# Kernel optimization log

Hardware: AMD Instinct MI355X
Metric: run time of the kernel (lower is better)

## Reference

```python
import jax, jax.numpy as jnp
import numpy as np
import math

B = 2048
NOSC = 64            # oscillators per modality
M = 3                # modalities (audio, text, vision) in sorted order
BDIM = 256           # binding_dim
DT = 0.01
NSTEPS = 10
DIMS = [512, 768, 1024]  # audio, text, vision
TWO_PI = 2.0 * math.pi


def setup_inputs() -> dict:
    key = jax.random.key(0)
    ks = iter(jax.random.split(key, 40))
    d = {}
    names = ['a', 't', 'v']
    for name, dim, x_key in zip(names, DIMS, ['x_audio', 'x_text', 'x_vision']):
        d[x_key] = jax.random.normal(next(ks), (B, dim), dtype=jnp.float32)
        s = 1.0 / math.sqrt(dim)
        d[f'Wf_{name}'] = jax.random.uniform(next(ks), (BDIM, dim), jnp.float32, -s, s)
        d[f'bf_{name}'] = jax.random.uniform(next(ks), (BDIM,), jnp.float32, -s, s)
        d[f'Wp_{name}'] = jax.random.uniform(next(ks), (NOSC, dim), jnp.float32, -s, s)
        d[f'bp_{name}'] = jax.random.uniform(next(ks), (NOSC,), jnp.float32, -s, s)
    # omegas: randn*0.1 + 1.0 + i*0.5 for i-th sorted modality
    for i, name in enumerate(names):
        d[f'omega_{name}'] = jax.random.normal(next(ks), (NOSC,), jnp.float32) * 0.1 + 1.0 + i * 0.5
    N = M * NOSC
    d['inter_coupling'] = jax.random.normal(next(ks), (N, N), jnp.float32) * 0.1
    s = 1.0 / math.sqrt(BDIM * M)
    d['W_fusion'] = jax.random.uniform(next(ks), (BDIM, BDIM * M), jnp.float32, -s, s)
    d['b_fusion'] = jax.random.uniform(next(ks), (BDIM,), jnp.float32, -s, s)
    return d


def reference(x_audio, x_text, x_vision,
              Wf_a, bf_a, Wp_a, bp_a,
              Wf_t, bf_t, Wp_t, bp_t,
              Wf_v, bf_v, Wp_v, bp_v,
              omega_a, omega_t, omega_v,
              inter_coupling, W_fusion, b_fusion):
    def enc(x, Wf, bf, Wp, bp):
        encoded = x @ Wf.T + bf                       # (B, BDIM)
        phases = (x @ Wp.T + bp) % TWO_PI             # (B, NOSC)
        return encoded, phases

    e_a, p_a = enc(x_audio, Wf_a, bf_a, Wp_a, bp_a)
    e_t, p_t = enc(x_text, Wf_t, bf_t, Wp_t, bp_t)
    e_v, p_v = enc(x_vision, Wf_v, bf_v, Wp_v, bp_v)

    phases = jnp.concatenate([p_a, p_t, p_v], axis=-1)        # (B, N)
    omega = jnp.concatenate([omega_a, omega_t, omega_v])      # (N,)
    K = (inter_coupling + inter_coupling.T) * 0.5             # (N, N)
    N = phases.shape[-1]

    def step(ph, _):
        diff = ph[:, :, None] - ph[:, None, :]                # (B, N, N)
        forces = jnp.einsum('ij,bij->bi', K, jnp.sin(diff)) / N
        ph = (ph + DT * (omega[None, :] + forces)) % TWO_PI
        return ph, None

    phases, _ = jax.lax.scan(step, phases, None, length=NSTEPS)

    pm = [phases[:, i * NOSC:(i + 1) * NOSC] for i in range(M)]  # per-modality

    # PLV between banks a,b: |mean_{i,j} exp(i(a_i - b_j))| = R_a * R_b where
    # R = |mean_k exp(i phi_k)| (resultant length), computed with real math.
    R = jnp.stack([jnp.sqrt(jnp.mean(jnp.cos(p), -1) ** 2 +
                            jnp.mean(jnp.sin(p), -1) ** 2) for p in pm])  # (M, B)
    bm = jnp.mean(R[:, None, :] * R[None, :, :], axis=-1)      # (M, M)
    binding_matrix = jnp.where(jnp.eye(M, dtype=bool), 1.0, bm)

    fused_parts = []
    for e, p in zip([e_a, e_t, e_v], pm):
        phase_mod = jnp.mean(jnp.cos(p), axis=-1, keepdims=True)  # (B, 1)
        fused_parts.append(e * (0.5 + 0.5 * phase_mod))
    fused = jnp.concatenate(fused_parts, axis=-1)              # (B, M*BDIM)
    bound = fused @ W_fusion.T + b_fusion                      # (B, BDIM)

    triu = jnp.triu(jnp.ones((M, M), dtype=bool), k=1)
    total = jnp.sum(jnp.where(triu, binding_matrix, 0.0)) / triu.sum()
    total_binding = jnp.full((bound.shape[0],), total)

    return bound, binding_matrix, phases, total_binding
```

## Files before the change

kernel.cpp:

```cpp
#include <hip/hip_runtime.h>
#include <math.h>

typedef short bf16x8 __attribute__((ext_vector_type(8)));
typedef short bf16x4 __attribute__((ext_vector_type(4)));
typedef float f32x4  __attribute__((ext_vector_type(4)));

#define INV_2PI  0.15915494309189535f
#define TWO_PI_F 6.283185307179586f
#define FSCALE   8.2893199e-06f

static __device__ inline short f2bf(float f) {
    union { float f; unsigned u; } v; v.f = f;
    unsigned r = (v.u + 0x7FFFu + ((v.u >> 16) & 1u)) >> 16;
    return (short)r;
}
static __device__ inline float bf2f(short h) {
    union { unsigned u; float f; } v; v.u = ((unsigned)(unsigned short)h) << 16;
    return v.f;
}

__global__ __launch_bounds__(256) void front_kernel(
    const float* __restrict__ xa, const float* __restrict__ xt, const float* __restrict__ xv,
    const float* __restrict__ Wpa, const float* __restrict__ Wpt, const float* __restrict__ Wpv,
    const float* __restrict__ Wfa, const float* __restrict__ Wft, const float* __restrict__ Wfv,
    const float* __restrict__ Wfu,
    const float* __restrict__ IC,
    const float* __restrict__ oa, const float* __restrict__ ot, const float* __restrict__ ov,
    const float* __restrict__ bpa, const float* __restrict__ bpt, const float* __restrict__ bpv,
    float* __restrict__ partial, short* __restrict__ XB, short* __restrict__ WB,
    short* __restrict__ Kp,
    float* __restrict__ om_eff, float* __restrict__ bp_all, float* __restrict__ bacc)
{
    __shared__ alignas(16) char smem[13056];
    int b = blockIdx.x;
    int t = threadIdx.x;

    if (b < 288) {
        float (*As)[136] = (float (*)[136])smem;
        float (*Bs)[68]  = (float (*)[68])(smem + 8704);
        int slot = b % 18, rb = b / 18;
        int z = slot < 4 ? 0 : (slot < 10 ? 1 : 2);
        int chunk = slot - (z == 0 ? 0 : (z == 1 ? 4 : 10));
        const float* A = z == 0 ? xa : (z == 1 ? xt : xv);
        const float* W = z == 0 ? Wpa : (z == 1 ? Wpt : Wpv);
        int K = z == 0 ? 512 : (z == 1 ? 768 : 1024);
        int kb = chunk * 128;
        int m0 = rb * 128;

        int tx = t & 15, ty = t >> 4;
        int c4 = t & 3, lr = t >> 2;

        float acc[8][4] = {};

        for (int k0 = 0; k0 < 128; k0 += 16) {
#pragma unroll
            for (int h = 0; h < 2; ++h) {
                int row = lr + 64 * h;
                float4 v = *(const float4*)&A[(size_t)(m0 + row) * K + kb + k0 + c4 * 4];
                As[c4 * 4 + 0][row] = v.x;
                As[c4 * 4 + 1][row] = v.y;
                As[c4 * 4 + 2][row] = v.z;
                As[c4 * 4 + 3][row] = v.w;
            }
            {
                int row = lr & 63;
                if (t < 256) {
                    float4 v = *(const float4*)&W[(size_t)row * K + kb + k0 + c4 * 4];
                    if (lr < 64) {
                        Bs[c4 * 4 + 0][row] = v.x;
                        Bs[c4 * 4 + 1][row] = v.y;
                        Bs[c4 * 4 + 2][row] = v.z;
                        Bs[c4 * 4 + 3][row] = v.w;
                    }
                }
            }
            __syncthreads();
#pragma unroll
            for (int kk = 0; kk < 16; ++kk) {
                float4 a0 = *(const float4*)&As[kk][ty * 8];
                float4 a1 = *(const float4*)&As[kk][ty * 8 + 4];
                float4 bq = *(const float4*)&Bs[kk][tx * 4];
                float av[8] = {a0.x, a0.y, a0.z, a0.w, a1.x, a1.y, a1.z, a1.w};
                float bv[4] = {bq.x, bq.y, bq.z, bq.w};
#pragma unroll
                for (int i = 0; i < 8; ++i)
#pragma unroll
                    for (int j = 0; j < 4; ++j)
                        acc[i][j] += av[i] * bv[j];
            }
            __syncthreads();
        }

        float* P = partial + (size_t)slot * 131072;
#pragma unroll
        for (int i = 0; i < 8; ++i) {
            float4 v = make_float4(acc[i][0], acc[i][1], acc[i][2], acc[i][3]);
            *(float4*)&P[(size_t)(m0 + ty * 8 + i) * 64 + tx * 4] = v;
        }
    } else if (b < 372) {
        for (int u = (b - 288) * 256 + t; u < 1376256; u += 84 * 256) {
            const float4* sp; short* dp;
            if (u < 262144)       { sp = (const float4*)xa  + u;            dp = XB + (size_t)u * 4; }
            else if (u < 655360)  { sp = (const float4*)xt  + (u - 262144); dp = XB + (size_t)u * 4; }
            else if (u < 1179648) { sp = (const float4*)xv  + (u - 655360); dp = XB + (size_t)u * 4; }
            else if (u < 1212416) { sp = (const float4*)Wfa + (u - 1179648); dp = WB + (size_t)(u - 1179648) * 4; }
            else if (u < 1261568) { sp = (const float4*)Wft + (u - 1212416); dp = WB + (size_t)(u - 1179648) * 4; }
            else if (u < 1327104) { sp = (const float4*)Wfv + (u - 1261568); dp = WB + (size_t)(u - 1179648) * 4; }
            else                  { sp = (const float4*)Wfu + (u - 1327104); dp = WB + (size_t)(u - 1179648) * 4; }
            float4 v = *sp;
            bf16x4 h; h[0] = f2bf(v.x); h[1] = f2bf(v.y); h[2] = f2bf(v.z); h[3] = f2bf(v.w);
            *(bf16x4*)dp = h;
        }
    } else if (b < 404) {
        for (int idx = (b - 372) * 256 + t; idx < 36864; idx += 32 * 256) {
            int k = idx / 192, n = idx - k * 192;
            float v = 0.5f * (IC[k * 192 + n] + IC[n * 192 + k]);
            int nt = n >> 4, kc = k >> 5;
            int lane = ((k >> 3) & 3) * 16 + (n & 15);
            int j = k & 7;
            Kp[((nt * 6 + kc) * 64 + lane) * 8 + j] = f2bf(v);
        }
    } else {
        if (t < 192) {
            float w = t < 64 ? oa[t] : (t < 128 ? ot[t - 64] : ov[t - 128]);
            om_eff[t] = w * (0.01f * INV_2PI);
            float bb = t < 64 ? bpa[t] : (t < 128 ? bpt[t - 64] : bpv[t - 128]);
            bp_all[t] = bb;
        }
        if (t < 4) bacc[t] = 0.f;
    }
}

__global__ __launch_bounds__(256) void mid_kernel(
    const short* __restrict__ XB, const short* __restrict__ WB,
    const float* __restrict__ ba, const float* __restrict__ bt, const float* __restrict__ bv,
    const float* __restrict__ partial, const float* __restrict__ bp_all,
    const short* __restrict__ Kp, const float* __restrict__ om_eff,
    short* __restrict__ e_bf16,
    float* __restrict__ phases_out, float* __restrict__ pm, float* __restrict__ bacc)
{
    __shared__ alignas(16) char smem[26816];
    int b = blockIdx.x;
    int t = threadIdx.x;
    int lane = t & 63, w = t >> 6;
    int q = lane >> 4, col = lane & 15;

    if (b < 384) {
        int z = b / 128, r = b % 128;
        int m0 = (r >> 2) * 64, n0 = (r & 3) * 64;
        const short* A    = XB + (z == 0 ? 0 : (z == 1 ? 1048576 : 2621440));
        const short* W    = WB + (z == 0 ? 0 : (z == 1 ? 131072 : 327680));
        const float* bias = z == 0 ? ba : (z == 1 ? bt : bv);
        int K             = z == 0 ? 512 : (z == 1 ? 768 : 1024);

        short* As = (short*)smem;
        short* Bs = (short*)smem + 64 * 72;

        f32x4 acc[4];
#pragma unroll
        for (int f = 0; f < 4; ++f)
#pragma unroll
            for (int rr = 0; rr < 4; ++rr) acc[f][rr] = 0.f;

        for (int kb = 0; kb < K; kb += 64) {
#pragma unroll
            for (int p = 0; p < 2; ++p) {
                int u = t + 256 * p;
                int row = u >> 3, c8 = u & 7;
                *(bf16x8*)&As[row * 72 + c8 * 8] = *(const bf16x8*)&A[(size_t)(m0 + row) * K + kb + c8 * 8];
                *(bf16x8*)&Bs[row * 72 + c8 * 8] = *(const bf16x8*)&W[(size_t)(n0 + row) * K + kb + c8 * 8];
            }
            __syncthreads();

            bf16x8 bfr[2];
#pragma unroll
            for (int kc = 0; kc < 2; ++kc)
                bfr[kc] = *(const bf16x8*)&Bs[(w * 16 + col) * 72 + kc * 32 + q * 8];
#pragma unroll
            for (int f = 0; f < 4; ++f)
#pragma unroll
                for (int kc = 0; kc < 2; ++kc) {
                    bf16x8 af = *(const bf16x8*)&As[(f * 16 + col) * 72 + kc * 32 + q * 8];
                    acc[f] = __builtin_amdgcn_mfma_f32_16x16x32_bf16(af, bfr[kc], acc[f], 0, 0, 0);
                }
            __syncthreads();
        }

        int n = n0 + w * 16 + col;
        float bn = bias[n];
#pragma unroll
        for (int f = 0; f < 4; ++f)
#pragma unroll
            for (int rr = 0; rr < 4; ++rr) {
                int m = m0 + f * 16 + q * 4 + rr;
                e_bf16[(size_t)m * 768 + z * 256 + n] = f2bf(acc[f][rr] + bn);
            }
    } else {
        short (*cs)[2][16][208] = (short (*)[2][16][208])smem;
        float (*Rl)[3] = (float (*)[3])(smem + 26624);

        int m0 = (b - 384) * 16;

        bf16x8 kb[3][6];
#pragma unroll
        for (int ntl = 0; ntl < 3; ++ntl)
#pragma unroll
            for (int kc = 0; kc < 6; ++kc) {
                int nt = w * 3 + ntl;
                kb[ntl][kc] = *(const bf16x8*)&Kp[((nt * 6 + kc) * 64 + lane) * 8];
            }

        float ph[3][4], om[3], c[3][4], s[3][4];
#pragma unroll
        for (int ntl = 0; ntl < 3; ++ntl) {
            int i = (w * 3 + ntl) * 16 + col;
            int z = i >> 6;
            int c0 = (z == 0) ? 0 : (z == 1 ? 4 : 10);
            int nch = (z == 0) ? 4 : (z == 1 ? 6 : 8);
            om[ntl] = om_eff[i];
#pragma unroll
            for (int r = 0; r < 4; ++r) {
                float raw = bp_all[i];
                size_t base = (size_t)c0 * 131072 + (size_t)(m0 + q * 4 + r) * 64 + (i & 63);
#pragma unroll
                for (int cc = 0; cc < 8; ++cc)
                    if (cc < nch) raw += partial[base + (size_t)cc * 131072];
                raw *= INV_2PI;
                ph[ntl][r] = raw - floorf(raw);
            }
        }

        for (int step = 0; step < 10; ++step) {
            int p = step & 1;
#pragma unroll
            for (int ntl = 0; ntl < 3; ++ntl) {
                int i = (w * 3 + ntl) * 16 + col;
#pragma unroll
                for (int r = 0; r < 4; ++r) {
                    c[ntl][r] = __builtin_amdgcn_cosf(ph[ntl][r]);
                    s[ntl][r] = __builtin_amdgcn_sinf(ph[ntl][r]);
                    cs[p][0][q * 4 + r][i] = f2bf(c[ntl][r]);
                    cs[p][1][q * 4 + r][i] = f2bf(s[ntl][r]);
                }
            }
            __syncthreads();

            f32x4 aC[3], aS[3];
#pragma unroll
            for (int ntl = 0; ntl < 3; ++ntl)
#pragma unroll
                for (int r = 0; r < 4; ++r) { aC[ntl][r] = 0.f; aS[ntl][r] = 0.f; }

#pragma unroll
            for (int kc = 0; kc < 6; ++kc) {
                bf16x8 ac  = *(const bf16x8*)&cs[p][0][col][kc * 32 + q * 8];
                bf16x8 as_ = *(const bf16x8*)&cs[p][1][col][kc * 32 + q * 8];
#pragma unroll
                for (int ntl = 0; ntl < 3; ++ntl) {
                    aC[ntl] = __builtin_amdgcn_mfma_f32_16x16x32_bf16(ac,  kb[ntl][kc], aC[ntl], 0, 0, 0);
                    aS[ntl] = __builtin_amdgcn_mfma_f32_16x16x32_bf16(as_, kb[ntl][kc], aS[ntl], 0, 0, 0);
                }
            }

#pragma unroll
            for (int ntl = 0; ntl < 3; ++ntl)
#pragma unroll
                for (int r = 0; r < 4; ++r) {
                    float f = (s[ntl][r] * aC[ntl][r] - c[ntl][r] * aS[ntl][r]) * FSCALE;
                    float pn = ph[ntl][r] + om[ntl] + f;
                    ph[ntl][r] = pn - floorf(pn);
                }
            if (step < 9) __syncthreads();
        }

        __syncthreads();
#pragma unroll
        for (int ntl = 0; ntl < 3; ++ntl) {
            int i = (w * 3 + ntl) * 16 + col;
#pragma unroll
            for (int r = 0; r < 4; ++r) {
                float cp = __builtin_amdgcn_cosf(ph[ntl][r]);
                float sp = __builtin_amdgcn_sinf(ph[ntl][r]);
                cs[0][0][q * 4 + r][i] = f2bf(cp);
                cs[0][1][q * 4 + r][i] = f2bf(sp);
                phases_out[(size_t)(m0 + q * 4 + r) * 192 + i] = ph[ntl][r] * TWO_PI_F;
            }
        }
        __syncthreads();

        if (t < 48) {
            int r = t & 15, mod = t >> 4;
            float sc = 0.f, ss = 0.f;
#pragma unroll
            for (int g = 0; g < 8; ++g) {
                bf16x8 vc = *(const bf16x8*)&cs[0][0][r][mod * 64 + g * 8];
                bf16x8 vs = *(const bf16x8*)&cs[0][1][r][mod * 64 + g * 8];
#pragma unroll
                for (int j = 0; j < 8; ++j) { sc += bf2f(vc[j]); ss += bf2f(vs[j]); }
            }
            sc *= (1.f / 64.f); ss *= (1.f / 64.f);
            pm[(size_t)(m0 + r) * 3 + mod] = 0.5f + 0.5f * sc;
            Rl[r][mod] = sqrtf(sc * sc + ss * ss);
        }
        __syncthreads();
        if (t < 3) {
            int a = (t == 2) ? 1 : 0;
            int bb = (t == 0) ? 1 : 2;
            float accp = 0.f;
            for (int r = 0; r < 16; ++r) accp += Rl[r][a] * Rl[r][bb];
            atomicAdd(&bacc[t], accp);
        }
    }
}

__global__ __launch_bounds__(256) void back_kernel(
    const short* __restrict__ e_bf16, const short* __restrict__ WB,
    const float* __restrict__ bias, const float* __restrict__ pm,
    const float* __restrict__ bacc,
    float* __restrict__ out_bound, float* __restrict__ out_bm, float* __restrict__ out_total)
{
    const short* Wfb = WB + 589824;
    int m0 = blockIdx.x * 64, n0 = blockIdx.y * 64;
    int t = threadIdx.x;
    int lane = t & 63, w = t >> 6;
    int q = lane >> 4, col = lane & 15;

    __shared__ alignas(16) short As[64 * 72];
    __shared__ alignas(16) short Bs[64 * 72];

    f32x4 acc[4];
#pragma unroll
    for (int f = 0; f < 4; ++f)
#pragma unroll
        for (int r = 0; r < 4; ++r) acc[f][r] = 0.f;

    for (int kb = 0; kb < 768; kb += 64) {
#pragma unroll
        for (int p = 0; p < 2; ++p) {
            int u = t + 256 * p;
            int row = u >> 3, c8 = u & 7;
            int k = kb + c8 * 8;
            int mod = k >> 8;
            bf16x8 v = *(const bf16x8*)&e_bf16[(size_t)(m0 + row) * 768 + k];
            float sc = pm[(size_t)(m0 + row) * 3 + mod];
            bf16x8 h;
#pragma unroll
            for (int j = 0; j < 8; ++j) h[j] = f2bf(bf2f(v[j]) * sc);
            *(bf16x8*)&As[row * 72 + c8 * 8] = h;

            *(bf16x8*)&Bs[row * 72 + c8 * 8] = *(const bf16x8*)&Wfb[(size_t)(n0 + row) * 768 + k];
        }
        __syncthreads();

        bf16x8 bfr[2];
#pragma unroll
        for (int kc = 0; kc < 2; ++kc)
            bfr[kc] = *(const bf16x8*)&Bs[(w * 16 + col) * 72 + kc * 32 + q * 8];
#pragma unroll
        for (int f = 0; f < 4; ++f)
#pragma unroll
            for (int kc = 0; kc < 2; ++kc) {
                bf16x8 af = *(const bf16x8*)&As[(f * 16 + col) * 72 + kc * 32 + q * 8];
                acc[f] = __builtin_amdgcn_mfma_f32_16x16x32_bf16(af, bfr[kc], acc[f], 0, 0, 0);
            }
        __syncthreads();
    }

    int n = n0 + w * 16 + col;
    float bn = bias[n];
#pragma unroll
    for (int f = 0; f < 4; ++f)
#pragma unroll
        for (int r = 0; r < 4; ++r) {
            int m = m0 + f * 16 + q * 4 + r;
            out_bound[(size_t)m * 256 + n] = acc[f][r] + bn;
        }

    if (blockIdx.x == 0 && blockIdx.y == 0) {
        float p01 = bacc[0] * (1.f / 2048.f);
        float p02 = bacc[1] * (1.f / 2048.f);
        float p12 = bacc[2] * (1.f / 2048.f);
        float total = (p01 + p02 + p12) * (1.f / 3.f);
        if (t == 0) {
            out_bm[0] = 1.f; out_bm[1] = p01; out_bm[2] = p02;
            out_bm[3] = p01; out_bm[4] = 1.f; out_bm[5] = p12;
            out_bm[6] = p02; out_bm[7] = p12; out_bm[8] = 1.f;
        }
        for (int i = t; i < 2048; i += 256) out_total[i] = total;
    }
}

extern "C" void kernel_launch(void* const* d_in, const int* in_sizes, int n_in,
                              void* d_out, int out_size, void* d_ws, size_t ws_size,
                              hipStream_t stream)
{
    const float* x_a  = (const float*)d_in[0];
    const float* Wf_a = (const float*)d_in[1];
    const float* bf_a = (const float*)d_in[2];
    const float* Wp_a = (const float*)d_in[3];
    const float* bp_a = (const float*)d_in[4];
    const float* x_t  = (const float*)d_in[5];
    const float* Wf_t = (const float*)d_in[6];
    const float* bf_t = (const float*)d_in[7];
    const float* Wp_t = (const float*)d_in[8];
    const float* bp_t = (const float*)d_in[9];
    const float* x_v  = (const float*)d_in[10];
    const float* Wf_v = (const float*)d_in[11];
    const float* bf_v = (const float*)d_in[12];
    const float* Wp_v = (const float*)d_in[13];
    const float* bp_v = (const float*)d_in[14];
    const float* om_a = (const float*)d_in[15];
    const float* om_t = (const float*)d_in[16];
    const float* om_v = (const float*)d_in[17];
    const float* IC   = (const float*)d_in[18];
    const float* Wfu  = (const float*)d_in[19];
    const float* bfu  = (const float*)d_in[20];

    float* ws      = (float*)d_ws;
    float* omw     = ws;
    float* bpw     = ws + 256;
    float* pmv     = ws + 512;
    float* baccw   = ws + 6656;
    float* partial = ws + 6720;
    short* e_bf    = (short*)(ws + 2366016);
    short* XB      = (short*)(ws + 3152448);
    short* WB      = (short*)(ws + 5511744);
    short* Kpck    = (short*)(ws + 5904960);

    float* out        = (float*)d_out;
    float* out_bound  = out;
    float* out_bm     = out + 524288;
    float* out_phases = out + 524297;
    float* out_total  = out + 917513;

    front_kernel<<<405, 256, 0, stream>>>(
        x_a, x_t, x_v, Wp_a, Wp_t, Wp_v, Wf_a, Wf_t, Wf_v, Wfu,
        IC, om_a, om_t, om_v, bp_a, bp_t, bp_v,
        partial, XB, WB, Kpck, omw, bpw, baccw);

    mid_kernel<<<512, 256, 0, stream>>>(
        XB, WB, bf_a, bf_t, bf_v,
        partial, bpw, Kpck, omw,
        e_bf, out_phases, pmv, baccw);

    dim3 gF(32, 4);
    back_kernel<<<gF, 256, 0, stream>>>(e_bf, WB, bfu, pmv, baccw,
                                        out_bound, out_bm, out_total);
}
```

Baseline: 176.8 us.

## Convert weights to bf16 in-GEMM, register-prefetch tiles, shrink tiles for more blocks

Stops pre-converting the fusion and encoder weights to bf16 in the front kernel. The mid and back GEMMs now load fp32 weights and convert them while staging into shared memory. All three GEMM loops prefetch the next K-tile into registers while the current tile is computed, which also removes one barrier per iteration. The phase GEMM and back GEMM use smaller M tiles, doubling their block counts for better occupancy. The cost is more fp32 weight traffic per block and extra conversion work inside the GEMMs.

Measured after the change: 168.1 us. 4.9% less time.

```diff
diff --git a/kernel.cpp b/kernel.cpp
--- a/kernel.cpp
+++ b/kernel.cpp
@@ -22,22 +22,18 @@
 __global__ __launch_bounds__(256) void front_kernel(
     const float* __restrict__ xa, const float* __restrict__ xt, const float* __restrict__ xv,
     const float* __restrict__ Wpa, const float* __restrict__ Wpt, const float* __restrict__ Wpv,
-    const float* __restrict__ Wfa, const float* __restrict__ Wft, const float* __restrict__ Wfv,
-    const float* __restrict__ Wfu,
     const float* __restrict__ IC,
     const float* __restrict__ oa, const float* __restrict__ ot, const float* __restrict__ ov,
     const float* __restrict__ bpa, const float* __restrict__ bpt, const float* __restrict__ bpv,
-    float* __restrict__ partial, short* __restrict__ XB, short* __restrict__ WB,
-    short* __restrict__ Kp,
+    float* __restrict__ partial, short* __restrict__ XB, short* __restrict__ Kp,
     float* __restrict__ om_eff, float* __restrict__ bp_all, float* __restrict__ bacc)
 {
-    __shared__ alignas(16) char smem[13056];
+    __shared__ alignas(16) float As[16][72];
+    __shared__ alignas(16) float Bs[16][72];
     int b = blockIdx.x;
     int t = threadIdx.x;
 
-    if (b < 288) {
-        float (*As)[136] = (float (*)[136])smem;
-        float (*Bs)[68]  = (float (*)[68])(smem + 8704);
+    if (b < 576) {
         int slot = b % 18, rb = b / 18;
         int z = slot < 4 ? 0 : (slot < 10 ? 1 : 2);
         int chunk = slot - (z == 0 ? 0 : (z == 1 ? 4 : 10));
@@ -45,74 +41,62 @@
         const float* W = z == 0 ? Wpa : (z == 1 ? Wpt : Wpv);
         int K = z == 0 ? 512 : (z == 1 ? 768 : 1024);
         int kb = chunk * 128;
-        int m0 = rb * 128;
+        int m0 = rb * 64;
 
         int tx = t & 15, ty = t >> 4;
-        int c4 = t & 3, lr = t >> 2;
-
-        float acc[8][4] = {};
+        int row = t >> 2, c4 = t & 3;
+
+        float acc[4][4] = {};
+        float4 ar = *(const float4*)&A[(size_t)(m0 + row) * K + kb + c4 * 4];
+        float4 br = *(const float4*)&W[(size_t)row * K + kb + c4 * 4];
 
         for (int k0 = 0; k0 < 128; k0 += 16) {
-#pragma unroll
-            for (int h = 0; h < 2; ++h) {
-                int row = lr + 64 * h;
-                float4 v = *(const float4*)&A[(size_t)(m0 + row) * K + kb + k0 + c4 * 4];
-                As[c4 * 4 + 0][row] = v.x;
-                As[c4 * 4 + 1][row] = v.y;
-                As[c4 * 4 + 2][row] = v.z;
-                As[c4 * 4 + 3][row] = v.w;
-            }
-            {
-                int row = lr & 63;
-                if (t < 256) {
-                    float4 v = *(const float4*)&W[(size_t)row * K + kb + k0 + c4 * 4];
-                    if (lr < 64) {
-                        Bs[c4 * 4 + 0][row] = v.x;
-                        Bs[c4 * 4 + 1][row] = v.y;
-                        Bs[c4 * 4 + 2][row] = v.z;
-                        Bs[c4 * 4 + 3][row] = v.w;
-                    }
-                }
-            }
+            if (k0) __syncthreads();
+            As[c4 * 4 + 0][row] = ar.x;
+            As[c4 * 4 + 1][row] = ar.y;
+            As[c4 * 4 + 2][row] = ar.z;
+            As[c4 * 4 + 3][row] = ar.w;
+            Bs[c4 * 4 + 0][row] = br.x;
+            Bs[c4 * 4 + 1][row] = br.y;
+            Bs[c4 * 4 + 2][row] = br.z;
+            Bs[c4 * 4 + 3][row] = br.w;
             __syncthreads();
+            if (k0 + 16 < 128) {
+                ar = *(const float4*)&A[(size_t)(m0 + row) * K + kb + k0 + 16 + c4 * 4];
+                br = *(const float4*)&W[(size_t)row * K + kb + k0 + 16 + c4 * 4];
+            }
 #pragma unroll
             for (int kk = 0; kk < 16; ++kk) {
-                float4 a0 = *(const float4*)&As[kk][ty * 8];
-                float4 a1 = *(const float4*)&As[kk][ty * 8 + 4];
+                float4 aq = *(const float4*)&As[kk][ty * 4];
                 float4 bq = *(const float4*)&Bs[kk][tx * 4];
-                float av[8] = {a0.x, a0.y, a0.z, a0.w, a1.x, a1.y, a1.z, a1.w};
+                float av[4] = {aq.x, aq.y, aq.z, aq.w};
                 float bv[4] = {bq.x, bq.y, bq.z, bq.w};
 #pragma unroll
-                for (int i = 0; i < 8; ++i)
+                for (int i = 0; i < 4; ++i)
 #pragma unroll
                     for (int j = 0; j < 4; ++j)
                         acc[i][j] += av[i] * bv[j];
             }
-            __syncthreads();
         }
 
         float* P = partial + (size_t)slot * 131072;
 #pragma unroll
-        for (int i = 0; i < 8; ++i) {
+        for (int i = 0; i < 4; ++i) {
             float4 v = make_float4(acc[i][0], acc[i][1], acc[i][2], acc[i][3]);
-            *(float4*)&P[(size_t)(m0 + ty * 8 + i) * 64 + tx * 4] = v;
-        }
-    } else if (b < 372) {
-        for (int u = (b - 288) * 256 + t; u < 1376256; u += 84 * 256) {
-            const float4* sp; short* dp;
-            if (u < 262144)       { sp = (const float4*)xa  + u;            dp = XB + (size_t)u * 4; }
-            else if (u < 655360)  { sp = (const float4*)xt  + (u - 262144); dp = XB + (size_t)u * 4; }
-            else if (u < 1179648) { sp = (const float4*)xv  + (u - 655360); dp = XB + (size_t)u * 4; }
-            else if (u < 1212416) { sp = (const float4*)Wfa + (u - 1179648); dp = WB + (size_t)(u - 1179648) * 4; }
-            else if (u < 1261568) { sp = (const float4*)Wft + (u - 1212416); dp = WB + (size_t)(u - 1179648) * 4; }
-            else if (u < 1327104) { sp = (const float4*)Wfv + (u - 1261568); dp = WB + (size_t)(u - 1179648) * 4; }
-            else                  { sp = (const float4*)Wfu + (u - 1327104); dp = WB + (size_t)(u - 1179648) * 4; }
+            *(float4*)&P[(size_t)(m0 + ty * 4 + i) * 64 + tx * 4] = v;
+        }
+    } else if (b < 648) {
+        for (int u = (b - 576) * 256 + t; u < 1179648; u += 72 * 256) {
+            const float4* sp;
+            if (u < 262144)      sp = (const float4*)xa + u;
+            else if (u < 655360) sp = (const float4*)xt + (u - 262144);
+            else                 sp = (const float4*)xv + (u - 655360);
             float4 v = *sp;
             bf16x4 h; h[0] = f2bf(v.x); h[1] = f2bf(v.y); h[2] = f2bf(v.z); h[3] = f2bf(v.w);
-            *(bf16x4*)dp = h;
-        }
-    } else if (b < 404) {
-        for (int idx = (b - 372) * 256 + t; idx < 36864; idx += 32 * 256) {
+            *(bf16x4*)(XB + (size_t)u * 4) = h;
+        }
+    } else if (b < 680) {
+        for (int idx = (b - 648) * 256 + t; idx < 36864; idx += 32 * 256) {
             int k = idx / 192, n = idx - k * 192;
             float v = 0.5f * (IC[k * 192 + n] + IC[n * 192 + k]);
             int nt = n >> 4, kc = k >> 5;
@@ -132,7 +116,8 @@
 }
 
 __global__ __launch_bounds__(256) void mid_kernel(
-    const short* __restrict__ XB, const short* __restrict__ WB,
+    const short* __restrict__ XB,
+    const float* __restrict__ Wfa, const float* __restrict__ Wft, const float* __restrict__ Wfv,
     const float* __restrict__ ba, const float* __restrict__ bt, const float* __restrict__ bv,
     const float* __restrict__ partial, const float* __restrict__ bp_all,
     const short* __restrict__ Kp, const float* __restrict__ om_eff,
@@ -149,7 +134,7 @@
         int z = b / 128, r = b % 128;
         int m0 = (r >> 2) * 64, n0 = (r & 3) * 64;
         const short* A    = XB + (z == 0 ? 0 : (z == 1 ? 1048576 : 2621440));
-        const short* W    = WB + (z == 0 ? 0 : (z == 1 ? 131072 : 327680));
+        const float* W    = z == 0 ? Wfa : (z == 1 ? Wft : Wfv);
         const float* bias = z == 0 ? ba : (z == 1 ? bt : bv);
         int K             = z == 0 ? 512 : (z == 1 ? 768 : 1024);
 
@@ -162,15 +147,53 @@
 #pragma unroll
             for (int rr = 0; rr < 4; ++rr) acc[f][rr] = 0.f;
 
+        bf16x8 av[2];
+#pragma unroll
+        for (int p = 0; p < 2; ++p) {
+            int u = t + 256 * p;
+            int arow = u >> 3, ac8 = u & 7;
+            av[p] = *(const bf16x8*)&A[(size_t)(m0 + arow) * K + ac8 * 8];
+        }
+        float4 bv4[4];
+#pragma unroll
+        for (int p = 0; p < 4; ++p) {
+            int u = t + 256 * p;
+            int brow = u >> 4, bc4 = u & 15;
+            bv4[p] = *(const float4*)&W[(size_t)(n0 + brow) * K + bc4 * 4];
+        }
+
         for (int kb = 0; kb < K; kb += 64) {
+            if (kb) __syncthreads();
 #pragma unroll
             for (int p = 0; p < 2; ++p) {
                 int u = t + 256 * p;
-                int row = u >> 3, c8 = u & 7;
-                *(bf16x8*)&As[row * 72 + c8 * 8] = *(const bf16x8*)&A[(size_t)(m0 + row) * K + kb + c8 * 8];
-                *(bf16x8*)&Bs[row * 72 + c8 * 8] = *(const bf16x8*)&W[(size_t)(n0 + row) * K + kb + c8 * 8];
+                int arow = u >> 3, ac8 = u & 7;
+                *(bf16x8*)&As[arow * 72 + ac8 * 8] = av[p];
+            }
+#pragma unroll
+            for (int p = 0; p < 4; ++p) {
+                int u = t + 256 * p;
+                int brow = u >> 4, bc4 = u & 15;
+                bf16x4 h;
+                h[0] = f2bf(bv4[p].x); h[1] = f2bf(bv4[p].y);
+                h[2] = f2bf(bv4[p].z); h[3] = f2bf(bv4[p].w);
+                *(bf16x4*)&Bs[brow * 72 + bc4 * 4] = h;
             }
             __syncthreads();
+            if (kb + 64 < K) {
+#pragma unroll
+                for (int p = 0; p < 2; ++p) {
+                    int u = t + 256 * p;
+                    int arow = u >> 3, ac8 = u & 7;
+                    av[p] = *(const bf16x8*)&A[(size_t)(m0 + arow) * K + kb + 64 + ac8 * 8];
+                }
+#pragma unroll
+                for (int p = 0; p < 4; ++p) {
+                    int u = t + 256 * p;
+                    int brow = u >> 4, bc4 = u & 15;
+                    bv4[p] = *(const float4*)&W[(size_t)(n0 + brow) * K + kb + 64 + bc4 * 4];
+                }
+            }
 
             bf16x8 bfr[2];
 #pragma unroll
@@ -183,7 +206,6 @@
                     bf16x8 af = *(const bf16x8*)&As[(f * 16 + col) * 72 + kc * 32 + q * 8];
                     acc[f] = __builtin_amdgcn_mfma_f32_16x16x32_bf16(af, bfr[kc], acc[f], 0, 0, 0);
                 }
-            __syncthreads();
         }
 
         int n = n0 + w * 16 + col;
@@ -314,62 +336,84 @@
 }
 
 __global__ __launch_bounds__(256) void back_kernel(
-    const short* __restrict__ e_bf16, const short* __restrict__ WB,
+    const short* __restrict__ e_bf16, const float* __restrict__ Wfu,
     const float* __restrict__ bias, const float* __restrict__ pm,
     const float* __restrict__ bacc,
     float* __restrict__ out_bound, float* __restrict__ out_bm, float* __restrict__ out_total)
 {
-    const short* Wfb = WB + 589824;
-    int m0 = blockIdx.x * 64, n0 = blockIdx.y * 64;
+    int m0 = blockIdx.x * 32, n0 = blockIdx.y * 64;
     int t = threadIdx.x;
     int lane = t & 63, w = t >> 6;
     int q = lane >> 4, col = lane & 15;
 
-    __shared__ alignas(16) short As[64 * 72];
+    __shared__ alignas(16) short As[32 * 72];
     __shared__ alignas(16) short Bs[64 * 72];
 
-    f32x4 acc[4];
-#pragma unroll
-    for (int f = 0; f < 4; ++f)
+    int arow = t >> 3, ac8 = t & 7;
+
+    f32x4 acc[2];
+#pragma unroll
+    for (int f = 0; f < 2; ++f)
 #pragma unroll
         for (int r = 0; r < 4; ++r) acc[f][r] = 0.f;
 
+    bf16x8 av = *(const bf16x8*)&e_bf16[(size_t)(m0 + arow) * 768 + ac8 * 8];
+    float asc = pm[(size_t)(m0 + arow) * 3 + 0];
+    float4 bv4[4];
+#pragma unroll
+    for (int p = 0; p < 4; ++p) {
+        int u = t + 256 * p;
+        int brow = u >> 4, bc4 = u & 15;
+        bv4[p] = *(const float4*)&Wfu[(size_t)(n0 + brow) * 768 + bc4 * 4];
+    }
+
     for (int kb = 0; kb < 768; kb += 64) {
-#pragma unroll
-        for (int p = 0; p < 2; ++p) {
+        if (kb) __syncthreads();
+        {
+            bf16x8 h;
+#pragma unroll
+            for (int j = 0; j < 8; ++j) h[j] = f2bf(bf2f(av[j]) * asc);
+            *(bf16x8*)&As[arow * 72 + ac8 * 8] = h;
+        }
+#pragma unroll
+        for (int p = 0; p < 4; ++p) {
             int u = t + 256 * p;
-            int row = u >> 3, c8 = u & 7;
-            int k = kb + c8 * 8;
-            int mod = k >> 8;
-            bf16x8 v = *(const bf16x8*)&e_bf16[(size_t)(m0 + row) * 768 + k];
-            float sc = pm[(size_t)(m0 + row) * 3 + mod];
-            bf16x8 h;
-#pragma unroll
-            for (int j = 0; j < 8; ++j) h[j] = f2bf(bf2f(v[j]) * sc);
-            *(bf16x8*)&As[row * 72 + c8 * 8] = h;
-
-            *(bf16x8*)&Bs[row * 72 + c8 * 8] = *(const bf16x8*)&Wfb[(size_t)(n0 + row) * 768 + k];
+            int brow = u >> 4, bc4 = u & 15;
+            bf16x4 h;
+            h[0] = f2bf(bv4[p].x); h[1] = f2bf(bv4[p].y);
+            h[2] = f2bf(bv4[p].z); h[3] = f2bf(bv4[p].w);
+            *(bf16x4*)&Bs[brow * 72 + bc4 * 4] = h;
         }
         __syncthreads();
+        if (kb + 64 < 768) {
+            int k = kb + 64;
+            av = *(const bf16x8*)&e_bf16[(size_t)(m0 + arow) * 768 + k + ac8 * 8];
+            asc = pm[(size_t)(m0 + arow) * 3 + (k >> 8)];
+#pragma unroll
+            for (int p = 0; p < 4; ++p) {
+                int u = t + 256 * p;
+                int brow = u >> 4, bc4 = u & 15;
+                bv4[p] = *(const float4*)&Wfu[(size_t)(n0 + brow) * 768 + k + bc4 * 4];
+            }
+        }
 
         bf16x8 bfr[2];
 #pragma unroll
         for (int kc = 0; kc < 2; ++kc)
             bfr[kc] = *(const bf16x8*)&Bs[(w * 16 + col) * 72 + kc * 32 + q * 8];
 #pragma unroll
-        for (int f = 0; f < 4; ++f)
+        for (int f = 0; f < 2; ++f)
 #pragma unroll
             for (int kc = 0; kc < 2; ++kc) {
                 bf16x8 af = *(const bf16x8*)&As[(f * 16 + col) * 72 + kc * 32 + q * 8];
                 acc[f] = __builtin_amdgcn_mfma_f32_16x16x32_bf16(af, bfr[kc], acc[f], 0, 0, 0);
             }
-        __syncthreads();
     }
 
     int n = n0 + w * 16 + col;
     float bn = bias[n];
 #pragma unroll
-    for (int f = 0; f < 4; ++f)
+    for (int f = 0; f < 2; ++f)
 #pragma unroll
         for (int r = 0; r < 4; ++r) {
             int m = m0 + f * 16 + q * 4 + r;
@@ -424,8 +468,7 @@
     float* partial = ws + 6720;
     short* e_bf    = (short*)(ws + 2366016);
     short* XB      = (short*)(ws + 3152448);
-    short* WB      = (short*)(ws + 5511744);
-    short* Kpck    = (short*)(ws + 5904960);
+    short* Kpck    = (short*)(ws + 5511744);
 
     float* out        = (float*)d_out;
     float* out_bound  = out;
@@ -433,17 +476,17 @@
     float* out_phases = out + 524297;
     float* out_total  = out + 917513;
 
-    front_kernel<<<405, 256, 0, stream>>>(
-        x_a, x_t, x_v, Wp_a, Wp_t, Wp_v, Wf_a, Wf_t, Wf_v, Wfu,
+    front_kernel<<<681, 256, 0, stream>>>(
+        x_a, x_t, x_v, Wp_a, Wp_t, Wp_v,
         IC, om_a, om_t, om_v, bp_a, bp_t, bp_v,
-        partial, XB, WB, Kpck, omw, bpw, baccw);
+        partial, XB, Kpck, omw, bpw, baccw);
 
     mid_kernel<<<512, 256, 0, stream>>>(
-        XB, WB, bf_a, bf_t, bf_v,
+        XB, Wf_a, Wf_t, Wf_v, bf_a, bf_t, bf_v,
         partial, bpw, Kpck, omw,
         e_bf, out_phases, pmv, baccw);
 
-    dim3 gF(32, 4);
-    back_kernel<<<gF, 256, 0, stream>>>(e_bf, WB, bfu, pmv, baccw,
+    dim3 gF(64, 4);
+    back_kernel<<<gF, 256, 0, stream>>>(e_bf, Wfu, bfu, pmv, baccw,
                                         out_bound, out_bm, out_total);
 }
```
